# Optimization experiments

Hardware: AMD Instinct MI355X
Metric: run time of the kernel (lower is better)

## Reference

```python
import jax, jax.numpy as jnp
import numpy as np

HIDDEN = 1024
HEADS = 16
D_K = HIDDEN // HEADS
B, S = 2, 2048


def setup_inputs() -> dict:
    key = jax.random.key(0)
    ks = jax.random.split(key, 11)
    sc = 1.0 / np.sqrt(HIDDEN)
    return {
        "query": jax.random.normal(ks[0], (B, S, HIDDEN), jnp.float32),
        "key": jax.random.normal(ks[1], (B, S, HIDDEN), jnp.float32),
        "value": jax.random.normal(ks[2], (B, S, HIDDEN), jnp.float32),
        "w_q": jax.random.normal(ks[3], (HIDDEN, HIDDEN), jnp.float32) * sc,
        "b_q": jax.random.normal(ks[4], (HIDDEN,), jnp.float32) * 0.02,
        "w_k": jax.random.normal(ks[5], (HIDDEN, HIDDEN), jnp.float32) * sc,
        "b_k": jax.random.normal(ks[6], (HIDDEN,), jnp.float32) * 0.02,
        "w_v": jax.random.normal(ks[7], (HIDDEN, HIDDEN), jnp.float32) * sc,
        "b_v": jax.random.normal(ks[8], (HIDDEN,), jnp.float32) * 0.02,
        "w_o": jax.random.normal(ks[9], (HIDDEN, HIDDEN), jnp.float32) * sc,
        "b_o": jax.random.normal(ks[10], (HIDDEN,), jnp.float32) * 0.02,
    }


def reference(query, key, value, w_q, b_q, w_k, b_k, w_v, b_v, w_o, b_o):
    b, s, _ = query.shape
    # linear projections (torch Linear: x @ W^T + b)
    q = query @ w_q.T + b_q
    k = key @ w_k.T + b_k
    v = value @ w_v.T + b_v
    # [B, H, S, D]
    q = q.reshape(b, s, HEADS, D_K).transpose(0, 2, 1, 3)
    k = k.reshape(b, s, HEADS, D_K).transpose(0, 2, 1, 3)
    v = v.reshape(b, s, HEADS, D_K).transpose(0, 2, 1, 3)
    scale = jnp.float32(1.0 / np.sqrt(D_K))
    scores = jnp.einsum('bhqd,bhkd->bhqk', q, k) * scale  # [B,H,S,S]
    probs = jax.nn.softmax(scores, axis=-1)
    y = jnp.einsum('bhqk,bhkd->bhqd', probs, v)
    y = y.transpose(0, 2, 1, 3).reshape(b, s, HIDDEN)
    return y @ w_o.T + b_o
```

## Files before the change

kernel.cpp:

```cpp
#include <hip/hip_runtime.h>
#include <hip/hip_bf16.h>
#include <math.h>

#define HIDDEN 1024
#define HEADS 16
#define DK 64
#define BB 2
#define SS 2048
#define MROWS (BB*SS)

typedef __attribute__((ext_vector_type(8))) short short8;
typedef __attribute__((ext_vector_type(4))) float f32x4;
typedef __attribute__((ext_vector_type(4))) unsigned short ushort4_t;

static __device__ __forceinline__ unsigned short f2bf(float f) {
    unsigned int u = __float_as_uint(f);
    u += 0x7fffu + ((u >> 16) & 1u);
    return (unsigned short)(u >> 16);
}

__global__ __launch_bounds__(256) void cast_all(
    const float* __restrict__ q, const float* __restrict__ k, const float* __restrict__ v,
    const float* __restrict__ wq, const float* __restrict__ wk,
    const float* __restrict__ wv, const float* __restrict__ wo,
    unsigned short* __restrict__ Xq, unsigned short* __restrict__ Xk, unsigned short* __restrict__ Xv,
    unsigned short* __restrict__ Wq, unsigned short* __restrict__ Wk,
    unsigned short* __restrict__ Wv, unsigned short* __restrict__ Wo) {
    int i = blockIdx.x * 256 + threadIdx.x;
    const float* src; unsigned short* dst; int off;
    if (i < (3 << 20)) {
        int w = i >> 20; off = i & ((1 << 20) - 1);
        src = (w == 0) ? q : (w == 1) ? k : v;
        dst = (w == 0) ? Xq : (w == 1) ? Xk : Xv;
    } else {
        int j = i - (3 << 20);
        int w = j >> 18; off = j & ((1 << 18) - 1);
        src = (w == 0) ? wq : (w == 1) ? wk : (w == 2) ? wv : wo;
        dst = (w == 0) ? Wq : (w == 1) ? Wk : (w == 2) ? Wv : Wo;
    }
    float4 f = reinterpret_cast<const float4*>(src)[off];
    ushort4_t o;
    o.x = f2bf(f.x); o.y = f2bf(f.y); o.z = f2bf(f.z); o.w = f2bf(f.w);
    reinterpret_cast<ushort4_t*>(dst)[off] = o;
}

__global__ __launch_bounds__(256, 3) void gemm_qkv(
    const unsigned short* __restrict__ Xq, const unsigned short* __restrict__ Xk, const unsigned short* __restrict__ Xv,
    const unsigned short* __restrict__ Wq, const unsigned short* __restrict__ Wk, const unsigned short* __restrict__ Wv,
    const float* __restrict__ bq, const float* __restrict__ bk, const float* __restrict__ bv,
    unsigned short* __restrict__ Qb, unsigned short* __restrict__ Kb, unsigned short* __restrict__ Vt,
    float scale_q) {
    __shared__ unsigned short As[128][40];
    __shared__ unsigned short Bs[128][40];
    const int z = blockIdx.z;
    const unsigned short* A  = (z == 0) ? Xq : (z == 1) ? Xk : Xv;
    const unsigned short* Wt = (z == 0) ? Wq : (z == 1) ? Wk : Wv;
    const float* bias        = (z == 0) ? bq : (z == 1) ? bk : bv;
    unsigned short* O        = (z == 0) ? Qb : (z == 1) ? Kb : Vt;
    const float oscale       = (z == 0) ? scale_q : 1.0f;

    const int t    = threadIdx.x;
    const int lane = t & 63;
    const int wave = t >> 6;
    const int m0 = blockIdx.y * 128;
    const int n0 = blockIdx.x * 128;
    const int row  = t >> 2;
    const int col8 = (t & 3) * 8;

    const int wm = (wave >> 1) * 64;
    const int wn = (wave & 1) * 64;
    const int lr = lane & 15;
    const int lk = (lane >> 4) * 8;

    f32x4 acc[4][4];
#pragma unroll
    for (int i = 0; i < 4; i++)
#pragma unroll
        for (int j = 0; j < 4; j++) acc[i][j] = f32x4{0.f, 0.f, 0.f, 0.f};

    for (int k0 = 0; k0 < HIDDEN; k0 += 32) {
        short8 av0 = *reinterpret_cast<const short8*>(A  + (size_t)(m0 + row)      * HIDDEN + k0 + col8);
        short8 av1 = *reinterpret_cast<const short8*>(A  + (size_t)(m0 + row + 64) * HIDDEN + k0 + col8);
        short8 bv0 = *reinterpret_cast<const short8*>(Wt + (size_t)(n0 + row)      * HIDDEN + k0 + col8);
        short8 bv1 = *reinterpret_cast<const short8*>(Wt + (size_t)(n0 + row + 64) * HIDDEN + k0 + col8);
        __syncthreads();
        *reinterpret_cast<short8*>(&As[row][col8])      = av0;
        *reinterpret_cast<short8*>(&As[row + 64][col8]) = av1;
        *reinterpret_cast<short8*>(&Bs[row][col8])      = bv0;
        *reinterpret_cast<short8*>(&Bs[row + 64][col8]) = bv1;
        __syncthreads();
        short8 af[4], bfr[4];
#pragma unroll
        for (int i = 0; i < 4; i++) af[i]  = *reinterpret_cast<const short8*>(&As[wm + i * 16 + lr][lk]);
#pragma unroll
        for (int j = 0; j < 4; j++) bfr[j] = *reinterpret_cast<const short8*>(&Bs[wn + j * 16 + lr][lk]);
#pragma unroll
        for (int i = 0; i < 4; i++)
#pragma unroll
            for (int j = 0; j < 4; j++)
                acc[i][j] = __builtin_amdgcn_mfma_f32_16x16x32_bf16(af[i], bfr[j], acc[i][j], 0, 0, 0);
    }

#pragma unroll
    for (int i = 0; i < 4; i++) {
        int mrow = m0 + wm + i * 16 + (lane >> 4) * 4;
#pragma unroll
        for (int j = 0; j < 4; j++) {
            int ncol = n0 + wn + j * 16 + lr;
            float bv = bias[ncol];
            int b_ = mrow >> 11;
            int h_ = ncol >> 6;
            int d_ = ncol & 63;
            if (z != 2) {
#pragma unroll
                for (int r = 0; r < 4; r++) {
                    int s_ = (mrow + r) & 2047;
                    O[(((size_t)(b_ * HEADS + h_)) * SS + s_) * DK + d_] = f2bf((acc[i][j][r] + bv) * oscale);
                }
            } else {
                int s0 = mrow & 2047;
                ushort4_t pk;
                pk.x = f2bf(acc[i][j][0] + bv);
                pk.y = f2bf(acc[i][j][1] + bv);
                pk.z = f2bf(acc[i][j][2] + bv);
                pk.w = f2bf(acc[i][j][3] + bv);
                *reinterpret_cast<ushort4_t*>(O + (((size_t)(b_ * HEADS + h_) * DK + d_) * SS + s0)) = pk;
            }
        }
    }
}

__global__ __launch_bounds__(256) void gemm_o(const unsigned short* __restrict__ A,
                                              const unsigned short* __restrict__ Wt,
                                              const float* __restrict__ bias,
                                              float* __restrict__ O) {
    __shared__ unsigned short As[128][40];
    __shared__ unsigned short Bs[64][40];
    const int t    = threadIdx.x;
    const int lane = t & 63;
    const int wave = t >> 6;
    const int m0 = blockIdx.y * 128;
    const int n0 = blockIdx.x * 64;
    const int row  = t >> 2;
    const int col8 = (t & 3) * 8;

    const int wm = wave * 32;
    const int lr = lane & 15;
    const int lk = (lane >> 4) * 8;

    f32x4 acc[2][4];
#pragma unroll
    for (int i = 0; i < 2; i++)
#pragma unroll
        for (int j = 0; j < 4; j++) acc[i][j] = f32x4{0.f, 0.f, 0.f, 0.f};

    for (int k0 = 0; k0 < HIDDEN; k0 += 32) {
        short8 av0 = *reinterpret_cast<const short8*>(A  + (size_t)(m0 + row)      * HIDDEN + k0 + col8);
        short8 av1 = *reinterpret_cast<const short8*>(A  + (size_t)(m0 + row + 64) * HIDDEN + k0 + col8);
        short8 bv0 = *reinterpret_cast<const short8*>(Wt + (size_t)(n0 + row)      * HIDDEN + k0 + col8);
        __syncthreads();
        *reinterpret_cast<short8*>(&As[row][col8])      = av0;
        *reinterpret_cast<short8*>(&As[row + 64][col8]) = av1;
        *reinterpret_cast<short8*>(&Bs[row][col8])      = bv0;
        __syncthreads();
        short8 af[2], bfr[4];
#pragma unroll
        for (int i = 0; i < 2; i++) af[i]  = *reinterpret_cast<const short8*>(&As[wm + i * 16 + lr][lk]);
#pragma unroll
        for (int j = 0; j < 4; j++) bfr[j] = *reinterpret_cast<const short8*>(&Bs[j * 16 + lr][lk]);
#pragma unroll
        for (int i = 0; i < 2; i++)
#pragma unroll
            for (int j = 0; j < 4; j++)
                acc[i][j] = __builtin_amdgcn_mfma_f32_16x16x32_bf16(af[i], bfr[j], acc[i][j], 0, 0, 0);
    }

#pragma unroll
    for (int i = 0; i < 2; i++) {
        int mrow = m0 + wm + i * 16 + (lane >> 4) * 4;
#pragma unroll
        for (int j = 0; j < 4; j++) {
            int ncol = n0 + j * 16 + lr;
            float bv = bias[ncol];
#pragma unroll
            for (int r = 0; r < 4; r++)
                O[(size_t)(mrow + r) * HIDDEN + ncol] = acc[i][j][r] + bv;
        }
    }
}

__global__ __launch_bounds__(256, 3) void attn_kernel(const unsigned short* __restrict__ Qb,
                                                      const unsigned short* __restrict__ Kb,
                                                      const unsigned short* __restrict__ Vt,
                                                      unsigned short* __restrict__ Yb) {
    __shared__ __attribute__((aligned(16))) unsigned short Ksh[2][64 * 64];
    __shared__ __attribute__((aligned(16))) unsigned short Vsh[2][64 * 64];
    __shared__ __attribute__((aligned(16))) unsigned short Psh[4][32][64];

    const int t    = threadIdx.x;
    const int lane = t & 63;
    const int wave = t >> 6;
    const int bh = blockIdx.y;
    const int b_ = bh >> 4, h_ = bh & 15;
    const int qbase = blockIdx.x * 128 + wave * 32;
    const unsigned short* Qp = Qb + (size_t)bh * SS * DK;
    const unsigned short* Kp = Kb + (size_t)bh * SS * DK;
    const unsigned short* Vp = Vt + (size_t)bh * DK * SS;
    const int lr = lane & 15;
    const int g  = lane >> 4;

    const int sr = lane >> 3;
    const int cs = (lane & 7) ^ sr;

    short8 bq[2][2];
#pragma unroll
    for (int qh = 0; qh < 2; qh++)
#pragma unroll
        for (int dh = 0; dh < 2; dh++)
            bq[qh][dh] = *reinterpret_cast<const short8*>(
                Qp + (size_t)(qbase + qh * 16 + lr) * DK + dh * 32 + g * 8);

    f32x4 accd[4][2];
#pragma unroll
    for (int dt = 0; dt < 4; dt++)
#pragma unroll
        for (int qh = 0; qh < 2; qh++) accd[dt][qh] = f32x4{0.f, 0.f, 0.f, 0.f};
    float mi[2] = {-INFINITY, -INFINITY};
    float li[2] = {0.f, 0.f};

#define STAGE(BUF, KV0) do {                                                                 \
    __builtin_amdgcn_global_load_lds(                                                        \
        (const __attribute__((address_space(1))) unsigned int*)(Kp + (size_t)((KV0) + wave * 16 + sr) * DK + cs * 8), \
        (__attribute__((address_space(3))) unsigned int*)&Ksh[BUF][(wave * 16) * 64], 16, 0, 0); \
    __builtin_amdgcn_global_load_lds(                                                        \
        (const __attribute__((address_space(1))) unsigned int*)(Kp + (size_t)((KV0) + wave * 16 + 8 + sr) * DK + cs * 8), \
        (__attribute__((address_space(3))) unsigned int*)&Ksh[BUF][(wave * 16 + 8) * 64], 16, 0, 0); \
    __builtin_amdgcn_global_load_lds(                                                        \
        (const __attribute__((address_space(1))) unsigned int*)(Vp + (size_t)(wave * 16 + sr) * SS + (KV0) + cs * 8), \
        (__attribute__((address_space(3))) unsigned int*)&Vsh[BUF][(wave * 16) * 64], 16, 0, 0); \
    __builtin_amdgcn_global_load_lds(                                                        \
        (const __attribute__((address_space(1))) unsigned int*)(Vp + (size_t)(wave * 16 + 8 + sr) * SS + (KV0) + cs * 8), \
        (__attribute__((address_space(3))) unsigned int*)&Vsh[BUF][(wave * 16 + 8) * 64], 16, 0, 0); \
} while (0)

    STAGE(0, 0);
    __syncthreads();

    for (int kv0 = 0; kv0 < SS; kv0 += 64) {
        const int cur = (kv0 >> 6) & 1;
        if (kv0 + 64 < SS) STAGE(cur ^ 1, kv0 + 64);

        short8 kf[4][2];
#pragma unroll
        for (int tt = 0; tt < 4; tt++)
#pragma unroll
            for (int h = 0; h < 2; h++)
                kf[tt][h] = *reinterpret_cast<const short8*>(
                    &Ksh[cur][(tt * 16 + lr) * 64 + (((h * 4 + g) ^ (lr & 7)) << 3)]);

        f32x4 sv[2][4];
#pragma unroll
        for (int qh = 0; qh < 2; qh++)
#pragma unroll
            for (int tt = 0; tt < 4; tt++) {
                f32x4 z = f32x4{0.f, 0.f, 0.f, 0.f};
                z = __builtin_amdgcn_mfma_f32_16x16x32_bf16(kf[tt][0], bq[qh][0], z, 0, 0, 0);
                z = __builtin_amdgcn_mfma_f32_16x16x32_bf16(kf[tt][1], bq[qh][1], z, 0, 0, 0);
                sv[qh][tt] = z;
            }

#pragma unroll
        for (int qh = 0; qh < 2; qh++) {
            float vmax = sv[qh][0][0];
#pragma unroll
            for (int tt = 0; tt < 4; tt++)
#pragma unroll
                for (int r = 0; r < 4; r++) vmax = fmaxf(vmax, sv[qh][tt][r]);
            vmax = fmaxf(vmax, __shfl_xor(vmax, 16));
            vmax = fmaxf(vmax, __shfl_xor(vmax, 32));
            if (!__all(vmax <= mi[qh] + 8.0f)) {
                float mnew = fmaxf(mi[qh], vmax);
                float sc = __builtin_amdgcn_exp2f(mi[qh] - mnew);
                li[qh] *= sc;
#pragma unroll
                for (int dt = 0; dt < 4; dt++)
#pragma unroll
                    for (int r = 0; r < 4; r++) accd[dt][qh][r] *= sc;
                mi[qh] = mnew;
            }
            float p[16];
            float rs = 0.f;
#pragma unroll
            for (int tt = 0; tt < 4; tt++)
#pragma unroll
                for (int r = 0; r < 4; r++) {
                    p[tt * 4 + r] = __builtin_amdgcn_exp2f(sv[qh][tt][r] - mi[qh]);
                    rs += p[tt * 4 + r];
                }
            rs += __shfl_xor(rs, 16);
            rs += __shfl_xor(rs, 32);
            li[qh] += rs;
#pragma unroll
            for (int tt = 0; tt < 4; tt++) {
                ushort4_t pk;
                pk.x = f2bf(p[tt * 4 + 0]);
                pk.y = f2bf(p[tt * 4 + 1]);
                pk.z = f2bf(p[tt * 4 + 2]);
                pk.w = f2bf(p[tt * 4 + 3]);
                int cw = (2 * tt + (g >> 1)) ^ (lr & 7);
                *reinterpret_cast<ushort4_t*>(&Psh[wave][qh * 16 + lr][cw * 8 + (g & 1) * 4]) = pk;
            }
        }

        __builtin_amdgcn_sched_barrier(0);

        short8 pf[2][2];
#pragma unroll
        for (int qh = 0; qh < 2; qh++)
#pragma unroll
            for (int h = 0; h < 2; h++)
                pf[qh][h] = *reinterpret_cast<const short8*>(
                    &Psh[wave][qh * 16 + lr][((h * 4 + g) ^ (lr & 7)) * 8]);

#pragma unroll
        for (int dt = 0; dt < 4; dt++) {
            short8 vf0 = *reinterpret_cast<const short8*>(
                &Vsh[cur][(dt * 16 + lr) * 64 + ((g ^ (lr & 7)) << 3)]);
            short8 vf1 = *reinterpret_cast<const short8*>(
                &Vsh[cur][(dt * 16 + lr) * 64 + (((4 + g) ^ (lr & 7)) << 3)]);
#pragma unroll
            for (int qh = 0; qh < 2; qh++) {
                accd[dt][qh] = __builtin_amdgcn_mfma_f32_16x16x32_bf16(vf0, pf[qh][0], accd[dt][qh], 0, 0, 0);
                accd[dt][qh] = __builtin_amdgcn_mfma_f32_16x16x32_bf16(vf1, pf[qh][1], accd[dt][qh], 0, 0, 0);
            }
        }
        __syncthreads();
    }
#undef STAGE

    float inv[2] = {1.0f / li[0], 1.0f / li[1]};
#pragma unroll
    for (int qh = 0; qh < 2; qh++) {
        size_t ob = ((size_t)b_ * SS + qbase + qh * 16 + lr) * HIDDEN + h_ * 64 + g * 4;
#pragma unroll
        for (int dt = 0; dt < 4; dt++) {
            ushort4_t o;
            o.x = f2bf(accd[dt][qh][0] * inv[qh]);
            o.y = f2bf(accd[dt][qh][1] * inv[qh]);
            o.z = f2bf(accd[dt][qh][2] * inv[qh]);
            o.w = f2bf(accd[dt][qh][3] * inv[qh]);
            *reinterpret_cast<ushort4_t*>(Yb + ob + dt * 16) = o;
        }
    }
}

extern "C" void kernel_launch(void* const* d_in, const int* in_sizes, int n_in,
                              void* d_out, int out_size, void* d_ws, size_t ws_size,
                              hipStream_t stream) {
    const float* query = (const float*)d_in[0];
    const float* key_  = (const float*)d_in[1];
    const float* value = (const float*)d_in[2];
    const float* w_q = (const float*)d_in[3];
    const float* b_q = (const float*)d_in[4];
    const float* w_k = (const float*)d_in[5];
    const float* b_k = (const float*)d_in[6];
    const float* w_v = (const float*)d_in[7];
    const float* b_v = (const float*)d_in[8];
    const float* w_o = (const float*)d_in[9];
    const float* b_o = (const float*)d_in[10];

    const size_t SZ_X = (size_t)MROWS * HIDDEN * 2;
    const size_t SZ_W = (size_t)HIDDEN * HIDDEN * 2;
    char* ws = (char*)d_ws;
    unsigned short* Xq = (unsigned short*)(ws);
    unsigned short* Xk = (unsigned short*)(ws + SZ_X);
    unsigned short* Xv = (unsigned short*)(ws + 2 * SZ_X);
    unsigned short* Wq = (unsigned short*)(ws + 3 * SZ_X);
    unsigned short* Wk = (unsigned short*)(ws + 3 * SZ_X + SZ_W);
    unsigned short* Wv = (unsigned short*)(ws + 3 * SZ_X + 2 * SZ_W);
    unsigned short* Wo = (unsigned short*)(ws + 3 * SZ_X + 3 * SZ_W);
    unsigned short* Qb = (unsigned short*)(ws + 3 * SZ_X + 4 * SZ_W);
    unsigned short* Kbf = (unsigned short*)(ws + 4 * SZ_X + 4 * SZ_W);
    unsigned short* Vt  = (unsigned short*)(ws + 5 * SZ_X + 4 * SZ_W);
    unsigned short* Yb  = (unsigned short*)(ws + 6 * SZ_X + 4 * SZ_W);

    cast_all<<<16384, 256, 0, stream>>>(query, key_, value, w_q, w_k, w_v, w_o,
                                        Xq, Xk, Xv, Wq, Wk, Wv, Wo);

    const float SCALE_Q = 0.125f * 1.4426950408889634f;
    gemm_qkv<<<dim3(HIDDEN / 128, MROWS / 128, 3), 256, 0, stream>>>(
        Xq, Xk, Xv, Wq, Wk, Wv, b_q, b_k, b_v, Qb, Kbf, Vt, SCALE_Q);

    attn_kernel<<<dim3(SS / 128, BB * HEADS), 256, 0, stream>>>(Qb, Kbf, Vt, Yb);

    gemm_o<<<dim3(HIDDEN / 64, MROWS / 128), 256, 0, stream>>>(Yb, Wo, b_o, (float*)d_out);
}
```

Before: 148.0 us.

## Fuse fp32-to-bf16 casts into GEMM loads and shrink attention query tile

Removes the separate cast kernel. The QKV and output-projection GEMMs now load fp32 inputs and weights directly and convert them to bf16 in registers with the packed v_cvt_pk_bf16_f32 instruction before the shared-memory store, which saves a full read/write pass over the activations and weights. The attention kernel now gives each wave 16 query rows instead of 32, launches twice as many blocks with higher occupancy bounds, and remaps block indices to change the scheduling order across heads. The trade-off is twice as many fp32 bytes read in the GEMM inner loops, and each K/V tile is reused by fewer queries in attention.

```diff
diff --git a/kernel.cpp b/kernel.cpp
--- a/kernel.cpp
+++ b/kernel.cpp
@@ -19,45 +19,34 @@
     return (unsigned short)(u >> 16);
 }
 
-__global__ __launch_bounds__(256) void cast_all(
-    const float* __restrict__ q, const float* __restrict__ k, const float* __restrict__ v,
-    const float* __restrict__ wq, const float* __restrict__ wk,
-    const float* __restrict__ wv, const float* __restrict__ wo,
-    unsigned short* __restrict__ Xq, unsigned short* __restrict__ Xk, unsigned short* __restrict__ Xv,
-    unsigned short* __restrict__ Wq, unsigned short* __restrict__ Wk,
-    unsigned short* __restrict__ Wv, unsigned short* __restrict__ Wo) {
-    int i = blockIdx.x * 256 + threadIdx.x;
-    const float* src; unsigned short* dst; int off;
-    if (i < (3 << 20)) {
-        int w = i >> 20; off = i & ((1 << 20) - 1);
-        src = (w == 0) ? q : (w == 1) ? k : v;
-        dst = (w == 0) ? Xq : (w == 1) ? Xk : Xv;
-    } else {
-        int j = i - (3 << 20);
-        int w = j >> 18; off = j & ((1 << 18) - 1);
-        src = (w == 0) ? wq : (w == 1) ? wk : (w == 2) ? wv : wo;
-        dst = (w == 0) ? Wq : (w == 1) ? Wk : (w == 2) ? Wv : Wo;
-    }
-    float4 f = reinterpret_cast<const float4*>(src)[off];
-    ushort4_t o;
-    o.x = f2bf(f.x); o.y = f2bf(f.y); o.z = f2bf(f.z); o.w = f2bf(f.w);
-    reinterpret_cast<ushort4_t*>(dst)[off] = o;
+static __device__ __forceinline__ unsigned int cvtpk(float lo, float hi) {
+    unsigned int r;
+    asm volatile("v_cvt_pk_bf16_f32 %0, %1, %2" : "=v"(r) : "v"(lo), "v"(hi));
+    return r;
+}
+static __device__ __forceinline__ short8 pack_bf16x8(float4 lo, float4 hi) {
+    union { unsigned int u[4]; short8 s; } r;
+    r.u[0] = cvtpk(lo.x, lo.y);
+    r.u[1] = cvtpk(lo.z, lo.w);
+    r.u[2] = cvtpk(hi.x, hi.y);
+    r.u[3] = cvtpk(hi.z, hi.w);
+    return r.s;
 }
 
 __global__ __launch_bounds__(256, 3) void gemm_qkv(
-    const unsigned short* __restrict__ Xq, const unsigned short* __restrict__ Xk, const unsigned short* __restrict__ Xv,
-    const unsigned short* __restrict__ Wq, const unsigned short* __restrict__ Wk, const unsigned short* __restrict__ Wv,
+    const float* __restrict__ Xq, const float* __restrict__ Xk, const float* __restrict__ Xv,
+    const float* __restrict__ Wq, const float* __restrict__ Wk, const float* __restrict__ Wv,
     const float* __restrict__ bq, const float* __restrict__ bk, const float* __restrict__ bv,
     unsigned short* __restrict__ Qb, unsigned short* __restrict__ Kb, unsigned short* __restrict__ Vt,
     float scale_q) {
     __shared__ unsigned short As[128][40];
     __shared__ unsigned short Bs[128][40];
     const int z = blockIdx.z;
-    const unsigned short* A  = (z == 0) ? Xq : (z == 1) ? Xk : Xv;
-    const unsigned short* Wt = (z == 0) ? Wq : (z == 1) ? Wk : Wv;
-    const float* bias        = (z == 0) ? bq : (z == 1) ? bk : bv;
-    unsigned short* O        = (z == 0) ? Qb : (z == 1) ? Kb : Vt;
-    const float oscale       = (z == 0) ? scale_q : 1.0f;
+    const float* A  = (z == 0) ? Xq : (z == 1) ? Xk : Xv;
+    const float* Wt = (z == 0) ? Wq : (z == 1) ? Wk : Wv;
+    const float* bias = (z == 0) ? bq : (z == 1) ? bk : bv;
+    unsigned short* O = (z == 0) ? Qb : (z == 1) ? Kb : Vt;
+    const float oscale = (z == 0) ? scale_q : 1.0f;
 
     const int t    = threadIdx.x;
     const int lane = t & 63;
@@ -79,15 +68,23 @@
         for (int j = 0; j < 4; j++) acc[i][j] = f32x4{0.f, 0.f, 0.f, 0.f};
 
     for (int k0 = 0; k0 < HIDDEN; k0 += 32) {
-        short8 av0 = *reinterpret_cast<const short8*>(A  + (size_t)(m0 + row)      * HIDDEN + k0 + col8);
-        short8 av1 = *reinterpret_cast<const short8*>(A  + (size_t)(m0 + row + 64) * HIDDEN + k0 + col8);
-        short8 bv0 = *reinterpret_cast<const short8*>(Wt + (size_t)(n0 + row)      * HIDDEN + k0 + col8);
-        short8 bv1 = *reinterpret_cast<const short8*>(Wt + (size_t)(n0 + row + 64) * HIDDEN + k0 + col8);
-        __syncthreads();
-        *reinterpret_cast<short8*>(&As[row][col8])      = av0;
-        *reinterpret_cast<short8*>(&As[row + 64][col8]) = av1;
-        *reinterpret_cast<short8*>(&Bs[row][col8])      = bv0;
-        *reinterpret_cast<short8*>(&Bs[row + 64][col8]) = bv1;
+        const float* a0 = A  + (size_t)(m0 + row) * HIDDEN + k0 + col8;
+        const float* a1 = A  + (size_t)(m0 + row + 64) * HIDDEN + k0 + col8;
+        const float* w0 = Wt + (size_t)(n0 + row) * HIDDEN + k0 + col8;
+        const float* w1 = Wt + (size_t)(n0 + row + 64) * HIDDEN + k0 + col8;
+        float4 a00 = reinterpret_cast<const float4*>(a0)[0];
+        float4 a01 = reinterpret_cast<const float4*>(a0)[1];
+        float4 a10 = reinterpret_cast<const float4*>(a1)[0];
+        float4 a11 = reinterpret_cast<const float4*>(a1)[1];
+        float4 w00 = reinterpret_cast<const float4*>(w0)[0];
+        float4 w01 = reinterpret_cast<const float4*>(w0)[1];
+        float4 w10 = reinterpret_cast<const float4*>(w1)[0];
+        float4 w11 = reinterpret_cast<const float4*>(w1)[1];
+        __syncthreads();
+        *reinterpret_cast<short8*>(&As[row][col8])      = pack_bf16x8(a00, a01);
+        *reinterpret_cast<short8*>(&As[row + 64][col8]) = pack_bf16x8(a10, a11);
+        *reinterpret_cast<short8*>(&Bs[row][col8])      = pack_bf16x8(w00, w01);
+        *reinterpret_cast<short8*>(&Bs[row + 64][col8]) = pack_bf16x8(w10, w11);
         __syncthreads();
         short8 af[4], bfr[4];
 #pragma unroll
@@ -131,7 +128,7 @@
 }
 
 __global__ __launch_bounds__(256) void gemm_o(const unsigned short* __restrict__ A,
-                                              const unsigned short* __restrict__ Wt,
+                                              const float* __restrict__ Wt,
                                               const float* __restrict__ bias,
                                               float* __restrict__ O) {
     __shared__ unsigned short As[128][40];
@@ -155,13 +152,15 @@
         for (int j = 0; j < 4; j++) acc[i][j] = f32x4{0.f, 0.f, 0.f, 0.f};
 
     for (int k0 = 0; k0 < HIDDEN; k0 += 32) {
-        short8 av0 = *reinterpret_cast<const short8*>(A  + (size_t)(m0 + row)      * HIDDEN + k0 + col8);
-        short8 av1 = *reinterpret_cast<const short8*>(A  + (size_t)(m0 + row + 64) * HIDDEN + k0 + col8);
-        short8 bv0 = *reinterpret_cast<const short8*>(Wt + (size_t)(n0 + row)      * HIDDEN + k0 + col8);
+        short8 av0 = *reinterpret_cast<const short8*>(A + (size_t)(m0 + row)      * HIDDEN + k0 + col8);
+        short8 av1 = *reinterpret_cast<const short8*>(A + (size_t)(m0 + row + 64) * HIDDEN + k0 + col8);
+        const float* w0 = Wt + (size_t)(n0 + row) * HIDDEN + k0 + col8;
+        float4 w00 = reinterpret_cast<const float4*>(w0)[0];
+        float4 w01 = reinterpret_cast<const float4*>(w0)[1];
         __syncthreads();
         *reinterpret_cast<short8*>(&As[row][col8])      = av0;
         *reinterpret_cast<short8*>(&As[row + 64][col8]) = av1;
-        *reinterpret_cast<short8*>(&Bs[row][col8])      = bv0;
+        *reinterpret_cast<short8*>(&Bs[row][col8])      = pack_bf16x8(w00, w01);
         __syncthreads();
         short8 af[2], bfr[4];
 #pragma unroll
@@ -189,20 +188,22 @@
     }
 }
 
-__global__ __launch_bounds__(256, 3) void attn_kernel(const unsigned short* __restrict__ Qb,
+__global__ __launch_bounds__(256, 4) void attn_kernel(const unsigned short* __restrict__ Qb,
                                                       const unsigned short* __restrict__ Kb,
                                                       const unsigned short* __restrict__ Vt,
                                                       unsigned short* __restrict__ Yb) {
     __shared__ __attribute__((aligned(16))) unsigned short Ksh[2][64 * 64];
     __shared__ __attribute__((aligned(16))) unsigned short Vsh[2][64 * 64];
-    __shared__ __attribute__((aligned(16))) unsigned short Psh[4][32][64];
+    __shared__ __attribute__((aligned(16))) unsigned short Psh[4][16][64];
 
     const int t    = threadIdx.x;
     const int lane = t & 63;
     const int wave = t >> 6;
-    const int bh = blockIdx.y;
+    const int fid  = blockIdx.y * gridDim.x + blockIdx.x;
+    const int qblk = (fid >> 3) & 31;
+    const int bh   = (fid & 7) * 4 + (fid >> 8);
     const int b_ = bh >> 4, h_ = bh & 15;
-    const int qbase = blockIdx.x * 128 + wave * 32;
+    const int qbase = qblk * 64 + wave * 16;
     const unsigned short* Qp = Qb + (size_t)bh * SS * DK;
     const unsigned short* Kp = Kb + (size_t)bh * SS * DK;
     const unsigned short* Vp = Vt + (size_t)bh * DK * SS;
@@ -212,21 +213,16 @@
     const int sr = lane >> 3;
     const int cs = (lane & 7) ^ sr;
 
-    short8 bq[2][2];
-#pragma unroll
-    for (int qh = 0; qh < 2; qh++)
-#pragma unroll
-        for (int dh = 0; dh < 2; dh++)
-            bq[qh][dh] = *reinterpret_cast<const short8*>(
-                Qp + (size_t)(qbase + qh * 16 + lr) * DK + dh * 32 + g * 8);
-
-    f32x4 accd[4][2];
-#pragma unroll
-    for (int dt = 0; dt < 4; dt++)
-#pragma unroll
-        for (int qh = 0; qh < 2; qh++) accd[dt][qh] = f32x4{0.f, 0.f, 0.f, 0.f};
-    float mi[2] = {-INFINITY, -INFINITY};
-    float li[2] = {0.f, 0.f};
+    short8 bq[2];
+#pragma unroll
+    for (int dh = 0; dh < 2; dh++)
+        bq[dh] = *reinterpret_cast<const short8*>(
+            Qp + (size_t)(qbase + lr) * DK + dh * 32 + g * 8);
+
+    f32x4 accd[4];
+#pragma unroll
+    for (int dt = 0; dt < 4; dt++) accd[dt] = f32x4{0.f, 0.f, 0.f, 0.f};
+    float mi = -INFINITY, li = 0.f;
 
 #define STAGE(BUF, KV0) do {                                                                 \
     __builtin_amdgcn_global_load_lds(                                                        \
@@ -258,69 +254,62 @@
                 kf[tt][h] = *reinterpret_cast<const short8*>(
                     &Ksh[cur][(tt * 16 + lr) * 64 + (((h * 4 + g) ^ (lr & 7)) << 3)]);
 
-        f32x4 sv[2][4];
-#pragma unroll
-        for (int qh = 0; qh < 2; qh++)
-#pragma unroll
-            for (int tt = 0; tt < 4; tt++) {
-                f32x4 z = f32x4{0.f, 0.f, 0.f, 0.f};
-                z = __builtin_amdgcn_mfma_f32_16x16x32_bf16(kf[tt][0], bq[qh][0], z, 0, 0, 0);
-                z = __builtin_amdgcn_mfma_f32_16x16x32_bf16(kf[tt][1], bq[qh][1], z, 0, 0, 0);
-                sv[qh][tt] = z;
+        f32x4 sv[4];
+#pragma unroll
+        for (int tt = 0; tt < 4; tt++) {
+            f32x4 z = f32x4{0.f, 0.f, 0.f, 0.f};
+            z = __builtin_amdgcn_mfma_f32_16x16x32_bf16(kf[tt][0], bq[0], z, 0, 0, 0);
+            z = __builtin_amdgcn_mfma_f32_16x16x32_bf16(kf[tt][1], bq[1], z, 0, 0, 0);
+            sv[tt] = z;
+        }
+
+        float vmax = sv[0][0];
+#pragma unroll
+        for (int tt = 0; tt < 4; tt++)
+#pragma unroll
+            for (int r = 0; r < 4; r++) vmax = fmaxf(vmax, sv[tt][r]);
+        vmax = fmaxf(vmax, __shfl_xor(vmax, 16));
+        vmax = fmaxf(vmax, __shfl_xor(vmax, 32));
+        if (!__all(vmax <= mi + 8.0f)) {
+            float mnew = fmaxf(mi, vmax);
+            float sc = __builtin_amdgcn_exp2f(mi - mnew);
+            li *= sc;
+#pragma unroll
+            for (int dt = 0; dt < 4; dt++)
+#pragma unroll
+                for (int r = 0; r < 4; r++) accd[dt][r] *= sc;
+            mi = mnew;
+        }
+        float p[16];
+        float rs = 0.f;
+#pragma unroll
+        for (int tt = 0; tt < 4; tt++)
+#pragma unroll
+            for (int r = 0; r < 4; r++) {
+                p[tt * 4 + r] = __builtin_amdgcn_exp2f(sv[tt][r] - mi);
+                rs += p[tt * 4 + r];
             }
-
-#pragma unroll
-        for (int qh = 0; qh < 2; qh++) {
-            float vmax = sv[qh][0][0];
-#pragma unroll
-            for (int tt = 0; tt < 4; tt++)
-#pragma unroll
-                for (int r = 0; r < 4; r++) vmax = fmaxf(vmax, sv[qh][tt][r]);
-            vmax = fmaxf(vmax, __shfl_xor(vmax, 16));
-            vmax = fmaxf(vmax, __shfl_xor(vmax, 32));
-            if (!__all(vmax <= mi[qh] + 8.0f)) {
-                float mnew = fmaxf(mi[qh], vmax);
-                float sc = __builtin_amdgcn_exp2f(mi[qh] - mnew);
-                li[qh] *= sc;
-#pragma unroll
-                for (int dt = 0; dt < 4; dt++)
-#pragma unroll
-                    for (int r = 0; r < 4; r++) accd[dt][qh][r] *= sc;
-                mi[qh] = mnew;
-            }
-            float p[16];
-            float rs = 0.f;
-#pragma unroll
-            for (int tt = 0; tt < 4; tt++)
-#pragma unroll
-                for (int r = 0; r < 4; r++) {
-                    p[tt * 4 + r] = __builtin_amdgcn_exp2f(sv[qh][tt][r] - mi[qh]);
-                    rs += p[tt * 4 + r];
-                }
-            rs += __shfl_xor(rs, 16);
-            rs += __shfl_xor(rs, 32);
-            li[qh] += rs;
-#pragma unroll
-            for (int tt = 0; tt < 4; tt++) {
-                ushort4_t pk;
-                pk.x = f2bf(p[tt * 4 + 0]);
-                pk.y = f2bf(p[tt * 4 + 1]);
-                pk.z = f2bf(p[tt * 4 + 2]);
-                pk.w = f2bf(p[tt * 4 + 3]);
-                int cw = (2 * tt + (g >> 1)) ^ (lr & 7);
-                *reinterpret_cast<ushort4_t*>(&Psh[wave][qh * 16 + lr][cw * 8 + (g & 1) * 4]) = pk;
-            }
+        rs += __shfl_xor(rs, 16);
+        rs += __shfl_xor(rs, 32);
+        li += rs;
+#pragma unroll
+        for (int tt = 0; tt < 4; tt++) {
+            ushort4_t pk;
+            pk.x = f2bf(p[tt * 4 + 0]);
+            pk.y = f2bf(p[tt * 4 + 1]);
+            pk.z = f2bf(p[tt * 4 + 2]);
+            pk.w = f2bf(p[tt * 4 + 3]);
+            int cw = (2 * tt + (g >> 1)) ^ (lr & 7);
+            *reinterpret_cast<ushort4_t*>(&Psh[wave][lr][cw * 8 + (g & 1) * 4]) = pk;
         }
 
         __builtin_amdgcn_sched_barrier(0);
 
-        short8 pf[2][2];
-#pragma unroll
-        for (int qh = 0; qh < 2; qh++)
-#pragma unroll
-            for (int h = 0; h < 2; h++)
-                pf[qh][h] = *reinterpret_cast<const short8*>(
-                    &Psh[wave][qh * 16 + lr][((h * 4 + g) ^ (lr & 7)) * 8]);
+        short8 pf[2];
+#pragma unroll
+        for (int h = 0; h < 2; h++)
+            pf[h] = *reinterpret_cast<const short8*>(
+                &Psh[wave][lr][((h * 4 + g) ^ (lr & 7)) * 8]);
 
 #pragma unroll
         for (int dt = 0; dt < 4; dt++) {
@@ -328,29 +317,23 @@
                 &Vsh[cur][(dt * 16 + lr) * 64 + ((g ^ (lr & 7)) << 3)]);
             short8 vf1 = *reinterpret_cast<const short8*>(
                 &Vsh[cur][(dt * 16 + lr) * 64 + (((4 + g) ^ (lr & 7)) << 3)]);
-#pragma unroll
-            for (int qh = 0; qh < 2; qh++) {
-                accd[dt][qh] = __builtin_amdgcn_mfma_f32_16x16x32_bf16(vf0, pf[qh][0], accd[dt][qh], 0, 0, 0);
-                accd[dt][qh] = __builtin_amdgcn_mfma_f32_16x16x32_bf16(vf1, pf[qh][1], accd[dt][qh], 0, 0, 0);
-            }
+            accd[dt] = __builtin_amdgcn_mfma_f32_16x16x32_bf16(vf0, pf[0], accd[dt], 0, 0, 0);
+            accd[dt] = __builtin_amdgcn_mfma_f32_16x16x32_bf16(vf1, pf[1], accd[dt], 0, 0, 0);
         }
         __syncthreads();
     }
 #undef STAGE
 
-    float inv[2] = {1.0f / li[0], 1.0f / li[1]};
-#pragma unroll
-    for (int qh = 0; qh < 2; qh++) {
-        size_t ob = ((size_t)b_ * SS + qbase + qh * 16 + lr) * HIDDEN + h_ * 64 + g * 4;
-#pragma unroll
-        for (int dt = 0; dt < 4; dt++) {
-            ushort4_t o;
-            o.x = f2bf(accd[dt][qh][0] * inv[qh]);
-            o.y = f2bf(accd[dt][qh][1] * inv[qh]);
-            o.z = f2bf(accd[dt][qh][2] * inv[qh]);
-            o.w = f2bf(accd[dt][qh][3] * inv[qh]);
-            *reinterpret_cast<ushort4_t*>(Yb + ob + dt * 16) = o;
-        }
+    float inv = 1.0f / li;
+    size_t ob = ((size_t)b_ * SS + qbase + lr) * HIDDEN + h_ * 64 + g * 4;
+#pragma unroll
+    for (int dt = 0; dt < 4; dt++) {
+        ushort4_t o;
+        o.x = f2bf(accd[dt][0] * inv);
+        o.y = f2bf(accd[dt][1] * inv);
+        o.z = f2bf(accd[dt][2] * inv);
+        o.w = f2bf(accd[dt][3] * inv);
+        *reinterpret_cast<ushort4_t*>(Yb + ob + dt * 16) = o;
     }
 }
 
@@ -370,28 +353,17 @@
     const float* b_o = (const float*)d_in[10];
 
     const size_t SZ_X = (size_t)MROWS * HIDDEN * 2;
-    const size_t SZ_W = (size_t)HIDDEN * HIDDEN * 2;
     char* ws = (char*)d_ws;
-    unsigned short* Xq = (unsigned short*)(ws);
-    unsigned short* Xk = (unsigned short*)(ws + SZ_X);
-    unsigned short* Xv = (unsigned short*)(ws + 2 * SZ_X);
-    unsigned short* Wq = (unsigned short*)(ws + 3 * SZ_X);
-    unsigned short* Wk = (unsigned short*)(ws + 3 * SZ_X + SZ_W);
-    unsigned short* Wv = (unsigned short*)(ws + 3 * SZ_X + 2 * SZ_W);
-    unsigned short* Wo = (unsigned short*)(ws + 3 * SZ_X + 3 * SZ_W);
-    unsigned short* Qb = (unsigned short*)(ws + 3 * SZ_X + 4 * SZ_W);
-    unsigned short* Kbf = (unsigned short*)(ws + 4 * SZ_X + 4 * SZ_W);
-    unsigned short* Vt  = (unsigned short*)(ws + 5 * SZ_X + 4 * SZ_W);
-    unsigned short* Yb  = (unsigned short*)(ws + 6 * SZ_X + 4 * SZ_W);
-
-    cast_all<<<16384, 256, 0, stream>>>(query, key_, value, w_q, w_k, w_v, w_o,
-                                        Xq, Xk, Xv, Wq, Wk, Wv, Wo);
+    unsigned short* Qb  = (unsigned short*)(ws);
+    unsigned short* Kbf = (unsigned short*)(ws + SZ_X);
+    unsigned short* Vt  = (unsigned short*)(ws + 2 * SZ_X);
+    unsigned short* Yb  = (unsigned short*)(ws + 3 * SZ_X);
 
     const float SCALE_Q = 0.125f * 1.4426950408889634f;
     gemm_qkv<<<dim3(HIDDEN / 128, MROWS / 128, 3), 256, 0, stream>>>(
-        Xq, Xk, Xv, Wq, Wk, Wv, b_q, b_k, b_v, Qb, Kbf, Vt, SCALE_Q);
-
-    attn_kernel<<<dim3(SS / 128, BB * HEADS), 256, 0, stream>>>(Qb, Kbf, Vt, Yb);
-
-    gemm_o<<<dim3(HIDDEN / 64, MROWS / 128), 256, 0, stream>>>(Yb, Wo, b_o, (float*)d_out);
-}
+        query, key_, value, w_q, w_k, w_v, b_q, b_k, b_v, Qb, Kbf, Vt, SCALE_Q);
+
+    attn_kernel<<<dim3(SS / 64, BB * HEADS), 256, 0, stream>>>(Qb, Kbf, Vt, Yb);
+
+    gemm_o<<<dim3(HIDDEN / 64, MROWS / 128), 256, 0, stream>>>(Yb, w_o, b_o, (float*)d_out);
+}
```

Result: slower. 156.6 us (+5.8%).
